# Kernel optimization log

Hardware: AMD Instinct MI355X
Metric: run time of the kernel (lower is better)

## Reference

```python
import jax, jax.numpy as jnp
import numpy as np

FEAT = 512
ACT_NUMS = (8, 6, 4)            # actions per categorical type
SUM_ACT = sum(ACT_NUMS)          # 18
STARTS = np.cumsum([0] + list(ACT_NUMS[:-1]))  # [0, 8, 14]
FC_HIDDEN, FC_OUT = 140, 256


def setup_inputs() -> dict:
    key = jax.random.key(0)
    ks = jax.random.split(key, 10)
    F, A = 2048, 32
    s = 0.02
    return {
        "current_feature": jax.random.normal(ks[0], (F, A, FEAT), jnp.float32),
        "next_feature": jax.random.normal(ks[1], (F, A, FEAT), jnp.float32),
        "actions": jax.random.randint(ks[2], (F, 3, A), 0, 4),
        "W1": jax.random.normal(ks[3], (FEAT + SUM_ACT, FC_HIDDEN), jnp.float32) * s,
        "b1": jnp.zeros((FC_HIDDEN,), jnp.float32),
        "W2": jax.random.normal(ks[4], (FC_HIDDEN, FC_OUT), jnp.float32) * s,
        "b2": jnp.zeros((FC_OUT,), jnp.float32),
        "Wi0": jax.random.normal(ks[5], (2 * FEAT, ACT_NUMS[0]), jnp.float32) * s,
        "bi0": jnp.zeros((ACT_NUMS[0],), jnp.float32),
        "Wi1": jax.random.normal(ks[6], (2 * FEAT, ACT_NUMS[1]), jnp.float32) * s,
        "bi1": jnp.zeros((ACT_NUMS[1],), jnp.float32),
        "Wi2": jax.random.normal(ks[7], (2 * FEAT, ACT_NUMS[2]), jnp.float32) * s,
        "bi2": jnp.zeros((ACT_NUMS[2],), jnp.float32),
    }


def reference(current_feature, next_feature, actions,
              W1, b1, W2, b2, Wi0, bi0, Wi1, bi1, Wi2, bi2):
    dt = current_feature.dtype
    starts = jnp.asarray(STARTS, dtype=actions.dtype)  # [3]
    # Vectorized replacement of the triple nested scatter loop:
    # global index per (frame, type, agent), one-hot over SUM_ACT, summed over types
    # (per-type index ranges are disjoint, so sum == set).
    idx = actions + starts[None, :, None]                       # [F, T, A]
    action_one_hot = jax.nn.one_hot(idx, SUM_ACT, dtype=dt).sum(axis=1)  # [F, A, S]

    # Forward dynamics: fwd_net = Linear -> Linear (no nonlinearity, per source)
    fwd_in = jnp.concatenate([current_feature, action_one_hot], axis=2)  # [F, A, FEAT+S]
    next_feature_pred = (fwd_in @ W1 + b1) @ W2 + b2                     # [F, A, 256]

    # Inverse dynamics: per-action-type Linear + Softmax(dim=1)
    # (nn.Softmax(dim=1) on a 3D tensor normalizes over the agent axis -- kept faithful)
    inv_in = jnp.concatenate([current_feature, next_feature], axis=2)    # [F, A, 2*FEAT]
    a0 = jax.nn.softmax(inv_in @ Wi0 + bi0, axis=1)
    a1 = jax.nn.softmax(inv_in @ Wi1 + bi1, axis=1)
    a2 = jax.nn.softmax(inv_in @ Wi2 + bi2, axis=1)
    return (next_feature_pred, a0, a1, a2)
```

## Files before the change

### kernel.cpp

```cpp
#include <hip/hip_runtime.h>


using bf16x8  = __attribute__((ext_vector_type(8))) __bf16;
using floatx4 = __attribute__((ext_vector_type(4))) float;

__device__ __forceinline__ unsigned short f2bf(float f) {
    unsigned int u = __float_as_uint(f);
    return (unsigned short)((u + 0x7fffu + ((u >> 16) & 1u)) >> 16);
}
__device__ __forceinline__ bf16x8 cvt8(const float* __restrict__ p) {
    float4 x = *(const float4*)p;
    float4 y = *(const float4*)(p + 4);
    union { bf16x8 v; unsigned short s[8]; } u;
    u.s[0] = f2bf(x.x); u.s[1] = f2bf(x.y); u.s[2] = f2bf(x.z); u.s[3] = f2bf(x.w);
    u.s[4] = f2bf(y.x); u.s[5] = f2bf(y.y); u.s[6] = f2bf(y.z); u.s[7] = f2bf(y.w);
    return u.v;
}

#define OFF_W1P 0
#define OFF_W2P (OFF_W1P + 16*9*512)
#define OFF_WCP (OFF_W2P + 5*16*512)

#define OFF_A0 ((size_t)16777216)
#define OFF_A1 ((size_t)17301504)
#define OFF_A2 ((size_t)17694720)

__global__ __launch_bounds__(256) void prep_kernel(
    const float* __restrict__ W1,
    const float* __restrict__ W2,
    const float* __restrict__ Wi0,
    const float* __restrict__ Wi1,
    const float* __restrict__ Wi2,
    unsigned short* __restrict__ ws)
{
    const int T1 = 16*9*512;
    const int T2 = T1 + 5*16*512;
    const int total = T2 + 32*2*512;
    for (int idx = blockIdx.x * 256 + threadIdx.x; idx < total; idx += gridDim.x * 256) {
        unsigned short v = 0;
        if (idx < T1) {
            int e = idx & 7, l = (idx >> 3) & 63;
            int n = (idx >> 9) % 9, kc = idx / (9*512);
            int k = kc*32 + ((l >> 4) << 3) + e, j = n*16 + (l & 15);
            if (j < 140) v = f2bf(W1[k*140 + j]);
            ws[OFF_W1P + idx] = v;
        } else if (idx < T2) {
            int i2 = idx - T1;
            int e = i2 & 7, l = (i2 >> 3) & 63;
            int n = (i2 >> 9) & 15, kc = i2 >> 13;
            int k = kc*32 + ((l >> 4) << 3) + e, j = n*16 + (l & 15);
            if (k < 140) v = f2bf(W2[k*256 + j]);
            ws[OFF_W2P + i2] = v;
        } else {
            int i3 = idx - T2;
            int e = i3 & 7, l = (i3 >> 3) & 63;
            int n = (i3 >> 9) & 1, kc = i3 >> 10;
            int k = kc*32 + ((l >> 4) << 3) + e, j = n*16 + (l & 15);
            if (j < 8)       v = f2bf(Wi0[k*8 + j]);
            else if (j < 14) v = f2bf(Wi1[k*6 + (j - 8)]);
            else if (j < 18) v = f2bf(Wi2[k*4 + (j - 14)]);
            ws[OFF_WCP + i3] = v;
        }
    }
}

__global__ __launch_bounds__(256) void fused_kernel(
    const float* __restrict__ cf,
    const float* __restrict__ nf,
    const int* __restrict__ actions,
    const float* __restrict__ W1,
    const float* __restrict__ b1,
    const float* __restrict__ b2,
    const unsigned short* __restrict__ ws,
    float* __restrict__ outp)
{
    __shared__ alignas(16) __bf16 hs[64 * 168];
    __shared__ float Us[18 * 144];
    __shared__ float b1s[144];
    __shared__ float b2s[256];
    __shared__ float Ls[64 * 20];
    __shared__ float rmx[36], rsc[36];
    __shared__ int   sidx[192];

    const int t = threadIdx.x, w = t >> 6, l = t & 63;
    const int m0 = blockIdx.x * 64;
    const int q = l >> 4, col = l & 15;
    const unsigned short* W1P = ws + OFF_W1P;
    const unsigned short* W2P = ws + OFF_W2P;
    const unsigned short* WCP = ws + OFF_WCP;

    for (int i = t; i < 18 * 144; i += 256) {
        int s = i / 144, j = i - s * 144;
        Us[i] = (j < 140) ? W1[(512 + s) * 140 + j] : 0.f;
    }
    if (t < 144) b1s[t] = (t < 140) ? b1[t] : 0.f;
    b2s[t] = b2[t];
    if (t < 192) {
        int r = t / 3, tt = t - r * 3;
        int m = m0 + r;
        int start = (tt == 0) ? 0 : (tt == 1 ? 8 : 14);
        sidx[t] = actions[(m >> 5) * 96 + tt * 32 + (m & 31)] + start;
    }

    const float* cfr = cf + (size_t)(m0 + w * 16 + col) * 512 + q * 8;
    const float* nfr = nf + (size_t)(m0 + w * 16 + col) * 512 + q * 8;

    floatx4 acc1[9], acc3[2];
#pragma unroll
    for (int n = 0; n < 9; ++n) { acc1[n][0]=0.f; acc1[n][1]=0.f; acc1[n][2]=0.f; acc1[n][3]=0.f; }
#pragma unroll
    for (int n = 0; n < 2; ++n) { acc3[n][0]=0.f; acc3[n][1]=0.f; acc3[n][2]=0.f; acc3[n][3]=0.f; }

    for (int kc = 0; kc < 16; ++kc) {
        bf16x8 av = cvt8(cfr + kc * 32);
        const unsigned short* bp = W1P + (size_t)(kc * 9) * 512 + l * 8;
#pragma unroll
        for (int n = 0; n < 9; ++n)
            acc1[n] = __builtin_amdgcn_mfma_f32_16x16x32_bf16(
                av, *(const bf16x8*)(bp + n * 512), acc1[n], 0, 0, 0);
        const unsigned short* cp = WCP + (size_t)(kc * 2) * 512 + l * 8;
        acc3[0] = __builtin_amdgcn_mfma_f32_16x16x32_bf16(
            av, *(const bf16x8*)(cp), acc3[0], 0, 0, 0);
        acc3[1] = __builtin_amdgcn_mfma_f32_16x16x32_bf16(
            av, *(const bf16x8*)(cp + 512), acc3[1], 0, 0, 0);
    }

    for (int kc = 0; kc < 16; ++kc) {
        bf16x8 av = cvt8(nfr + kc * 32);
        const unsigned short* cp = WCP + (size_t)((16 + kc) * 2) * 512 + l * 8;
        acc3[0] = __builtin_amdgcn_mfma_f32_16x16x32_bf16(
            av, *(const bf16x8*)(cp), acc3[0], 0, 0, 0);
        acc3[1] = __builtin_amdgcn_mfma_f32_16x16x32_bf16(
            av, *(const bf16x8*)(cp + 512), acc3[1], 0, 0, 0);
    }

    __syncthreads();

    const int r0 = w * 16 + (q << 2);
#pragma unroll
    for (int i = 0; i < 4; ++i) {
        int rr = r0 + i;
        int s0 = sidx[rr * 3], s1 = sidx[rr * 3 + 1], s2 = sidx[rr * 3 + 2];
#pragma unroll
        for (int n = 0; n < 9; ++n) {
            int j = n * 16 + col;
            float v = acc1[n][i] + b1s[j] + Us[s0 * 144 + j] + Us[s1 * 144 + j] + Us[s2 * 144 + j];
            ((unsigned short*)hs)[rr * 168 + j] = f2bf(v);
        }
    }
    {
        int rr = t >> 2, g = t & 3;
        ushort4 z; z.x = z.y = z.z = z.w = 0;
        *(ushort4*)((unsigned short*)hs + rr * 168 + 144 + g * 4) = z;
    }
    __syncthreads();

    floatx4 acc2[16];
#pragma unroll
    for (int n = 0; n < 16; ++n) { acc2[n][0]=0.f; acc2[n][1]=0.f; acc2[n][2]=0.f; acc2[n][3]=0.f; }

    for (int kc = 0; kc < 5; ++kc) {
        bf16x8 av = *(const bf16x8*)&hs[(w * 16 + col) * 168 + kc * 32 + q * 8];
        const unsigned short* bp = W2P + (size_t)(kc * 16) * 512 + l * 8;
#pragma unroll
        for (int n = 0; n < 16; ++n)
            acc2[n] = __builtin_amdgcn_mfma_f32_16x16x32_bf16(
                av, *(const bf16x8*)(bp + n * 512), acc2[n], 0, 0, 0);
    }
#pragma unroll
    for (int n = 0; n < 16; ++n) {
        int j = n * 16 + col;
        float bj = b2s[j];
#pragma unroll
        for (int i = 0; i < 4; ++i)
            outp[(size_t)(m0 + r0 + i) * 256 + j] = acc2[n][i] + bj;
    }

#pragma unroll
    for (int n = 0; n < 2; ++n) {
        int j = n * 16 + col;
        if (j < 18) {
#pragma unroll
            for (int i = 0; i < 4; ++i) Ls[(r0 + i) * 20 + j] = acc3[n][i];
        }
    }
    __syncthreads();

    if (t < 36) {
        int fr = t / 18, j = t - fr * 18;
        float mx = -1e30f;
        for (int a = 0; a < 32; ++a) mx = fmaxf(mx, Ls[(fr * 32 + a) * 20 + j]);
        float s = 0.f;
        for (int a = 0; a < 32; ++a) s += expf(Ls[(fr * 32 + a) * 20 + j] - mx);
        rmx[t] = mx; rsc[t] = 1.f / s;
    }
    __syncthreads();

#pragma unroll
    for (int it = 0; it < 5; ++it) {
        int idx = t + it * 256;
        if (idx < 1152) {
            int r = idx / 18, j = idx - r * 18;
            int fr = r >> 5;
            float v = expf(Ls[r * 20 + j] - rmx[fr * 18 + j]) * rsc[fr * 18 + j];
            int m = m0 + r;
            size_t o;
            if (j < 8)       o = OFF_A0 + (size_t)m * 8 + j;
            else if (j < 14) o = OFF_A1 + (size_t)m * 6 + (j - 8);
            else             o = OFF_A2 + (size_t)m * 4 + (j - 14);
            outp[o] = v;
        }
    }
}

extern "C" void kernel_launch(void* const* d_in, const int* in_sizes, int n_in,
                              void* d_out, int out_size, void* d_ws, size_t ws_size,
                              hipStream_t stream)
{
    const float* cf  = (const float*)d_in[0];
    const float* nf  = (const float*)d_in[1];
    const int*   act = (const int*)d_in[2];
    const float* W1  = (const float*)d_in[3];
    const float* b1  = (const float*)d_in[4];
    const float* W2  = (const float*)d_in[5];
    const float* b2  = (const float*)d_in[6];
    const float* Wi0 = (const float*)d_in[7];
    const float* Wi1 = (const float*)d_in[9];
    const float* Wi2 = (const float*)d_in[11];

    unsigned short* ws = (unsigned short*)d_ws;
    float* outp = (float*)d_out;

    hipLaunchKernelGGL(prep_kernel, dim3(144), dim3(256), 0, stream,
                       W1, W2, Wi0, Wi1, Wi2, ws);
    hipLaunchKernelGGL(fused_kernel, dim3(1024), dim3(256), 0, stream,
                       cf, nf, act, W1, b1, b2, ws, outp);
}
```

Baseline: 389.2 us.

## Prefetch activation chunks, stagger K order per block, batch prologue loads

The K loops over current and next features now load the next 32-float chunk before converting and multiplying the current one. Each block starts at a different K offset (blockIdx mod 16), which spreads accesses to the packed weight workspace across blocks. Prologue global loads for the action-row weights, biases and action indices are gathered into registers before any shared-memory store, so their latencies overlap. The logits store into shared memory moves ahead of an existing barrier, removing one __syncthreads. These add register pressure and may lower occupancy.

```diff
diff --git a/kernel.cpp b/kernel.cpp
--- a/kernel.cpp
+++ b/kernel.cpp
@@ -8,9 +8,7 @@
     unsigned int u = __float_as_uint(f);
     return (unsigned short)((u + 0x7fffu + ((u >> 16) & 1u)) >> 16);
 }
-__device__ __forceinline__ bf16x8 cvt8(const float* __restrict__ p) {
-    float4 x = *(const float4*)p;
-    float4 y = *(const float4*)(p + 4);
+__device__ __forceinline__ bf16x8 cvt8r(float4 x, float4 y) {
     union { bf16x8 v; unsigned short s[8]; } u;
     u.s[0] = f2bf(x.x); u.s[1] = f2bf(x.y); u.s[2] = f2bf(x.z); u.s[3] = f2bf(x.w);
     u.s[4] = f2bf(y.x); u.s[5] = f2bf(y.y); u.s[6] = f2bf(y.z); u.s[7] = f2bf(y.w);
@@ -89,17 +87,34 @@
     const unsigned short* W2P = ws + OFF_W2P;
     const unsigned short* WCP = ws + OFF_WCP;
 
-    for (int i = t; i < 18 * 144; i += 256) {
-        int s = i / 144, j = i - s * 144;
-        Us[i] = (j < 140) ? W1[(512 + s) * 140 + j] : 0.f;
-    }
-    if (t < 144) b1s[t] = (t < 140) ? b1[t] : 0.f;
-    b2s[t] = b2[t];
-    if (t < 192) {
-        int r = t / 3, tt = t - r * 3;
-        int m = m0 + r;
-        int start = (tt == 0) ? 0 : (tt == 1 ? 8 : 14);
-        sidx[t] = actions[(m >> 5) * 96 + tt * 32 + (m & 31)] + start;
+    {
+        float uv[11];
+#pragma unroll
+        for (int it = 0; it < 11; ++it) {
+            int i = t + it * 256;
+            uv[it] = 0.f;
+            if (i < 18 * 144) {
+                int s = i / 144, j = i - s * 144;
+                if (j < 140) uv[it] = W1[(512 + s) * 140 + j];
+            }
+        }
+        float bv1 = (t < 140) ? b1[t] : 0.f;
+        float bv2 = b2[t];
+        int sv = 0;
+        if (t < 192) {
+            int r = t / 3, tt = t - r * 3;
+            int m = m0 + r;
+            int start = (tt == 0) ? 0 : (tt == 1 ? 8 : 14);
+            sv = actions[(m >> 5) * 96 + tt * 32 + (m & 31)] + start;
+        }
+#pragma unroll
+        for (int it = 0; it < 11; ++it) {
+            int i = t + it * 256;
+            if (i < 18 * 144) Us[i] = uv[it];
+        }
+        if (t < 144) b1s[t] = bv1;
+        b2s[t] = bv2;
+        if (t < 192) sidx[t] = sv;
     }
 
     const float* cfr = cf + (size_t)(m0 + w * 16 + col) * 512 + q * 8;
@@ -111,27 +126,47 @@
 #pragma unroll
     for (int n = 0; n < 2; ++n) { acc3[n][0]=0.f; acc3[n][1]=0.f; acc3[n][2]=0.f; acc3[n][3]=0.f; }
 
-    for (int kc = 0; kc < 16; ++kc) {
-        bf16x8 av = cvt8(cfr + kc * 32);
-        const unsigned short* bp = W1P + (size_t)(kc * 9) * 512 + l * 8;
-#pragma unroll
-        for (int n = 0; n < 9; ++n)
-            acc1[n] = __builtin_amdgcn_mfma_f32_16x16x32_bf16(
-                av, *(const bf16x8*)(bp + n * 512), acc1[n], 0, 0, 0);
-        const unsigned short* cp = WCP + (size_t)(kc * 2) * 512 + l * 8;
-        acc3[0] = __builtin_amdgcn_mfma_f32_16x16x32_bf16(
-            av, *(const bf16x8*)(cp), acc3[0], 0, 0, 0);
-        acc3[1] = __builtin_amdgcn_mfma_f32_16x16x32_bf16(
-            av, *(const bf16x8*)(cp + 512), acc3[1], 0, 0, 0);
-    }
-
-    for (int kc = 0; kc < 16; ++kc) {
-        bf16x8 av = cvt8(nfr + kc * 32);
-        const unsigned short* cp = WCP + (size_t)((16 + kc) * 2) * 512 + l * 8;
-        acc3[0] = __builtin_amdgcn_mfma_f32_16x16x32_bf16(
-            av, *(const bf16x8*)(cp), acc3[0], 0, 0, 0);
-        acc3[1] = __builtin_amdgcn_mfma_f32_16x16x32_bf16(
-            av, *(const bf16x8*)(cp + 512), acc3[1], 0, 0, 0);
+    const int base = blockIdx.x & 15;
+
+    {
+        float4 c0 = *(const float4*)(cfr + base * 32);
+        float4 c1 = *(const float4*)(cfr + base * 32 + 4);
+        for (int i = 0; i < 16; ++i) {
+            const int kc  = (base + i) & 15;
+            const int kn  = (base + i + 1) & 15;
+            float4 n0 = *(const float4*)(cfr + kn * 32);
+            float4 n1 = *(const float4*)(cfr + kn * 32 + 4);
+            bf16x8 av = cvt8r(c0, c1);
+            const unsigned short* bp = W1P + (size_t)(kc * 9) * 512 + l * 8;
+#pragma unroll
+            for (int n = 0; n < 9; ++n)
+                acc1[n] = __builtin_amdgcn_mfma_f32_16x16x32_bf16(
+                    av, *(const bf16x8*)(bp + n * 512), acc1[n], 0, 0, 0);
+            const unsigned short* cp = WCP + (size_t)(kc * 2) * 512 + l * 8;
+            acc3[0] = __builtin_amdgcn_mfma_f32_16x16x32_bf16(
+                av, *(const bf16x8*)(cp), acc3[0], 0, 0, 0);
+            acc3[1] = __builtin_amdgcn_mfma_f32_16x16x32_bf16(
+                av, *(const bf16x8*)(cp + 512), acc3[1], 0, 0, 0);
+            c0 = n0; c1 = n1;
+        }
+    }
+
+    {
+        float4 c0 = *(const float4*)(nfr + base * 32);
+        float4 c1 = *(const float4*)(nfr + base * 32 + 4);
+        for (int i = 0; i < 16; ++i) {
+            const int kc  = (base + i) & 15;
+            const int kn  = (base + i + 1) & 15;
+            float4 n0 = *(const float4*)(nfr + kn * 32);
+            float4 n1 = *(const float4*)(nfr + kn * 32 + 4);
+            bf16x8 av = cvt8r(c0, c1);
+            const unsigned short* cp = WCP + (size_t)((16 + kc) * 2) * 512 + l * 8;
+            acc3[0] = __builtin_amdgcn_mfma_f32_16x16x32_bf16(
+                av, *(const bf16x8*)(cp), acc3[0], 0, 0, 0);
+            acc3[1] = __builtin_amdgcn_mfma_f32_16x16x32_bf16(
+                av, *(const bf16x8*)(cp + 512), acc3[1], 0, 0, 0);
+            c0 = n0; c1 = n1;
+        }
     }
 
     __syncthreads();
@@ -153,6 +188,14 @@
         ushort4 z; z.x = z.y = z.z = z.w = 0;
         *(ushort4*)((unsigned short*)hs + rr * 168 + 144 + g * 4) = z;
     }
+#pragma unroll
+    for (int n = 0; n < 2; ++n) {
+        int j = n * 16 + col;
+        if (j < 18) {
+#pragma unroll
+            for (int i = 0; i < 4; ++i) Ls[(r0 + i) * 20 + j] = acc3[n][i];
+        }
+    }
     __syncthreads();
 
     floatx4 acc2[16];
@@ -175,16 +218,6 @@
         for (int i = 0; i < 4; ++i)
             outp[(size_t)(m0 + r0 + i) * 256 + j] = acc2[n][i] + bj;
     }
-
-#pragma unroll
-    for (int n = 0; n < 2; ++n) {
-        int j = n * 16 + col;
-        if (j < 18) {
-#pragma unroll
-            for (int i = 0; i < 4; ++i) Ls[(r0 + i) * 20 + j] = acc3[n][i];
-        }
-    }
-    __syncthreads();
 
     if (t < 36) {
         int fr = t / 18, j = t - fr * 18;
```

Result: faster. 364.5 us (-6.3%).
